# Optimization experiments

Hardware: AMD Instinct MI355X
Metric: run time of the kernel (lower is better)

## Reference

```python
import jax, jax.numpy as jnp
import numpy as np

N = 100000      # nodes
E = 1600000     # edges
D_IN = 128
D_H = 128
D_OUT = 128


def setup_inputs() -> dict:
    key = jax.random.key(0)
    ks = jax.random.split(key, 8)
    x = jax.random.normal(ks[0], (N, D_IN), dtype=jnp.float32)
    edge_index = jax.random.randint(ks[1], (2, E), 0, N, dtype=jnp.int32)
    s = 1.0 / np.sqrt(D_IN)
    W1 = jax.random.uniform(ks[2], (D_IN, D_H), jnp.float32, -s, s)
    b1 = jnp.zeros((D_H,), jnp.float32)
    W2 = jax.random.uniform(ks[3], (D_H, D_H), jnp.float32, -s, s)
    b2 = jnp.zeros((D_H,), jnp.float32)
    W3 = jax.random.uniform(ks[4], (D_H, D_OUT), jnp.float32, -s, s)
    b3 = jnp.zeros((D_OUT,), jnp.float32)
    return {"x": x, "edge_index": edge_index,
            "W1": W1, "b1": b1, "W2": W2, "b2": b2, "W3": W3, "b3": b3}


def _gcn_conv(x, W, b, src, dst, norm, n_nodes):
    # PyG GCNConv: out = scatter_add(norm * (x @ W)[src] -> dst) + b
    h = x @ W
    msg = h[src] * norm[:, None]                       # [E+N, d]
    agg = jax.ops.segment_sum(msg, dst, num_segments=n_nodes)
    return agg + b


def reference(x, edge_index, W1, b1, W2, b2, W3, b3):
    n = x.shape[0]
    loop = jnp.arange(n, dtype=edge_index.dtype)
    src = jnp.concatenate([edge_index[0], loop])       # add self-loops
    dst = jnp.concatenate([edge_index[1], loop])
    # symmetric normalization: deg computed on target (incl. self-loops)
    deg = jax.ops.segment_sum(jnp.ones_like(dst, dtype=x.dtype), dst,
                              num_segments=n)
    dis = jnp.where(deg > 0, jax.lax.rsqrt(jnp.maximum(deg, 1.0)), 0.0)
    norm = dis[src] * dis[dst]                         # [E+N]

    h = _gcn_conv(x, W1, b1, src, dst, norm, n)
    h = jax.nn.relu(h)                                 # dropout: eval mode = identity
    h = _gcn_conv(h, W2, b2, src, dst, norm, n)
    h = jax.nn.relu(h)
    out = _gcn_conv(h, W3, b3, src, dst, norm, n)
    return out
```

## Files before the change

### kernel.cpp

```cpp
#include <hip/hip_runtime.h>
#include <hip/hip_fp16.h>

#define D 128
#define TPAD 136
#define NPB 256
#define KMAX 512
#define CHUNK 4096
#define SCAP 6144
#define SRCMASK 0x1FFFF

typedef _Float16 half_t;
typedef _Float16 f16x8 __attribute__((ext_vector_type(8)));
typedef float f32x4 __attribute__((ext_vector_type(4)));


__global__ __launch_bounds__(256) void setup_kernel(const float* __restrict__ W1,
                                                    const float* __restrict__ W2,
                                                    const float* __restrict__ W3,
                                                    half_t* __restrict__ Wf1,
                                                    half_t* __restrict__ Wf2,
                                                    half_t* __restrict__ Wf3,
                                                    const int* __restrict__ dst,
                                                    int* __restrict__ bucket_cnt, int E) {
    __shared__ int scnt[KMAX];
    int b = blockIdx.x, t = threadIdx.x;
    if (b < 96) {
        const float* W = (b < 32) ? W1 : (b < 64) ? W2 : W3;
        half_t* Wf = (b < 32) ? Wf1 : (b < 64) ? Wf2 : Wf3;
        int bb = b & 31;
        int s = bb >> 3, tq = bb & 7;
        for (int e = t; e < 512; e += 256) {
            int l = e >> 3, j = e & 7;
            int k = s * 32 + ((l >> 4) & 3) * 4 + (j & 3) + ((j >> 2) << 4);
            int nn = tq * 16 + (l & 15);
            Wf[(size_t)((s * 8 + tq) * 64 + l) * 8 + j] = (half_t)W[k * 128 + nn];
        }
    } else if (b >= 98) {
        for (int i = t; i < KMAX; i += 256) scnt[i] = 0;
        __syncthreads();
        int base = (b - 98) * CHUNK;
        int nE = min(CHUNK, E - base);
        for (int i = t; i < nE; i += 256)
            atomicAdd(&scnt[dst[base + i] >> 8], 1);
        __syncthreads();
        for (int i = t; i < KMAX; i += 256)
            if (scnt[i]) atomicAdd(&bucket_cnt[i], scnt[i]);
    }
}

__global__ __launch_bounds__(KMAX) void bucket_scan_kernel(const int* __restrict__ bucket_cnt,
                                                           int* __restrict__ bucket_ptr,
                                                           int* __restrict__ bucket_cur,
                                                           int K, int E) {
    __shared__ int sh[KMAX];
    int t = threadIdx.x;
    int v = (t < K) ? bucket_cnt[t] : 0;
    sh[t] = v;
    __syncthreads();
    for (int off = 1; off < KMAX; off <<= 1) {
        int add = (t >= off) ? sh[t - off] : 0;
        __syncthreads();
        sh[t] += add;
        __syncthreads();
    }
    if (t < K) {
        int ex = sh[t] - v;
        bucket_ptr[t] = ex;
        bucket_cur[t] = ex;
    }
    if (t == 0) bucket_ptr[K] = E;
}

__global__ __launch_bounds__(256) void bucket_scatter_kernel(const int* __restrict__ src,
                                                             const int* __restrict__ dst,
                                                             int* __restrict__ bucket_cur,
                                                             int* __restrict__ bpack, int E) {
    __shared__ int sdst[CHUNK];
    __shared__ int scnt[KMAX];
    __shared__ int sbase[KMAX];
    int t = threadIdx.x;
    int base = blockIdx.x * CHUNK;
    int nE = min(CHUNK, E - base);
    for (int i = t; i < KMAX; i += 256) scnt[i] = 0;
    __syncthreads();
    for (int i = t; i < nE; i += 256) {
        int d = dst[base + i];
        sdst[i] = d;
        atomicAdd(&scnt[d >> 8], 1);
    }
    __syncthreads();
    for (int i = t; i < KMAX; i += 256) {
        int c = scnt[i];
        sbase[i] = c ? atomicAdd(&bucket_cur[i], c) : 0;
        scnt[i] = 0;
    }
    __syncthreads();
    for (int i = t; i < nE; i += 256) {
        int d = sdst[i];
        int b = d >> 8;
        int pos = sbase[b] + atomicAdd(&scnt[b], 1);
        bpack[pos] = src[base + i] | ((d & 255) << 17);
    }
}

__global__ __launch_bounds__(256) void csr_build_kernel(const int* __restrict__ bpack,
                                                        const int* __restrict__ bucket_ptr,
                                                        int* __restrict__ row_ptr,
                                                        float* __restrict__ dis,
                                                        int* __restrict__ csr_src,
                                                        int n, int E, int K) {
    __shared__ int scnt[NPB];
    __shared__ int sh[NPB];
    __shared__ int sedge[SCAP];
    int b = blockIdx.x;
    int node0 = b << 8;
    int nn = min(NPB, n - node0);
    int t = threadIdx.x;
    int p0 = bucket_ptr[b], p1 = bucket_ptr[b + 1];
    int cnt = p1 - p0;
    bool stage = (cnt <= SCAP);
    scnt[t] = 0;
    __syncthreads();
    for (int i = t; i < cnt; i += 256) {
        int e = bpack[p0 + i];
        if (stage) sedge[i] = e;
        atomicAdd(&scnt[(e >> 17) & 255], 1);
    }
    __syncthreads();
    int v = scnt[t];
    sh[t] = v;
    __syncthreads();
    for (int off = 1; off < NPB; off <<= 1) {
        int add = (t >= off) ? sh[t - off] : 0;
        __syncthreads();
        sh[t] += add;
        __syncthreads();
    }
    int rowbase = p0 + sh[t] - v;
    if (t < nn) {
        row_ptr[node0 + t] = rowbase;
        dis[node0 + t] = rsqrtf((float)(v + 1));
    }
    if (b == K - 1 && t == 0) row_ptr[n] = E;
    scnt[t] = rowbase;
    __syncthreads();
    for (int i = t; i < cnt; i += 256) {
        int e = stage ? sedge[i] : bpack[p0 + i];
        int pos = atomicAdd(&scnt[(e >> 17) & 255], 1);
        csr_src[pos] = e & SRCMASK;
    }
}


__device__ __forceinline__ void gemm_core(half_t* sA, int tid, int base,
                                          const half_t* __restrict__ Wf,
                                          const float* __restrict__ dis,
                                          half_t* __restrict__ C, int n) {
    int l = tid & 63, w = tid >> 6;
    int m = l & 15, g = l >> 4;
    const f16x8* WF = (const f16x8*)Wf;

    f16x8 wB[4][2];
#pragma unroll
    for (int s = 0; s < 4; ++s)
#pragma unroll
        for (int j = 0; j < 2; ++j)
            wB[s][j] = WF[(size_t)(s * 8 + 2 * w + j) * 64 + l];

    f32x4 acc[4][2];
#pragma unroll
    for (int rt = 0; rt < 4; ++rt)
#pragma unroll
        for (int j = 0; j < 2; ++j) acc[rt][j] = (f32x4){0.f, 0.f, 0.f, 0.f};

#pragma unroll
    for (int s = 0; s < 4; ++s) {
#pragma unroll
        for (int rt = 0; rt < 4; ++rt) {
            union { f16x8 v; float2 f2[2]; } af;
            int a_off = (rt * 16 + m) * TPAD + s * 32 + 4 * g;
            af.f2[0] = *(const float2*)&sA[a_off];
            af.f2[1] = *(const float2*)&sA[a_off + 16];
            acc[rt][0] = __builtin_amdgcn_mfma_f32_16x16x32_f16(af.v, wB[s][0], acc[rt][0], 0, 0, 0);
            acc[rt][1] = __builtin_amdgcn_mfma_f32_16x16x32_f16(af.v, wB[s][1], acc[rt][1], 0, 0, 0);
        }
    }

    float dd[4][4];
#pragma unroll
    for (int rt = 0; rt < 4; ++rt)
#pragma unroll
        for (int r = 0; r < 4; ++r) {
            int row = base + rt * 16 + 4 * g + r;
            dd[rt][r] = (row < n) ? dis[row] : 0.f;
        }
    __syncthreads();
#pragma unroll
    for (int rt = 0; rt < 4; ++rt)
#pragma unroll
        for (int j = 0; j < 2; ++j)
#pragma unroll
            for (int r = 0; r < 4; ++r)
                sA[(rt * 16 + 4 * g + r) * TPAD + (2 * w + j) * 16 + m] =
                    (half_t)(acc[rt][j][r] * dd[rt][r]);
    __syncthreads();
#pragma unroll
    for (int q = 0; q < 4; ++q) {
        int f4 = q * 256 + tid;
        int r = f4 >> 4, c = f4 & 15;
        int row = base + r;
        if (row < n)
            *(float4*)&C[(size_t)row * D + c * 8] = *(const float4*)&sA[r * TPAD + c * 8];
    }
}

__global__ __launch_bounds__(256) void gemm_mfma_f32in(const float* __restrict__ A,
                                                       const half_t* __restrict__ Wf,
                                                       const float* __restrict__ dis,
                                                       half_t* __restrict__ C, int n) {
    __shared__ half_t sA[64 * TPAD];
    int tid = threadIdx.x;
    int base = blockIdx.x * 64;

    const float4* A4 = (const float4*)A;
#pragma unroll
    for (int it = 0; it < 8; ++it) {
        int idx = it * 256 + tid;
        int r = idx >> 5, kq = idx & 31;
        int grow = base + r;
        float4 va = (grow < n) ? A4[(size_t)grow * 32 + kq]
                               : make_float4(0.f, 0.f, 0.f, 0.f);
        union { half_t h[4]; float2 f2; } pk;
        pk.h[0] = (half_t)va.x; pk.h[1] = (half_t)va.y;
        pk.h[2] = (half_t)va.z; pk.h[3] = (half_t)va.w;
        *(float2*)&sA[r * TPAD + kq * 4] = pk.f2;
    }
    __syncthreads();
    gemm_core(sA, tid, base, Wf, dis, C, n);
}

__global__ __launch_bounds__(256) void gemm_mfma_f16in(const half_t* __restrict__ A,
                                                       const half_t* __restrict__ Wf,
                                                       const float* __restrict__ dis,
                                                       half_t* __restrict__ C, int n) {
    __shared__ half_t sA[64 * TPAD];
    int tid = threadIdx.x;
    int base = blockIdx.x * 64;

    const float4* A4 = (const float4*)A;
#pragma unroll
    for (int it = 0; it < 4; ++it) {
        int idx = it * 256 + tid;
        int r = idx >> 4, c16 = idx & 15;
        int grow = base + r;
        float4 va = (grow < n) ? A4[(size_t)grow * 16 + c16]
                               : make_float4(0.f, 0.f, 0.f, 0.f);
        *(float4*)&sA[r * TPAD + c16 * 8] = va;
    }
    __syncthreads();
    gemm_core(sA, tid, base, Wf, dis, C, n);
}


template <bool F16OUT>
__global__ __launch_bounds__(256) void aggregate_kernel(const __half2* __restrict__ Hs,
                                                        const int* __restrict__ row_ptr,
                                                        const int* __restrict__ csr_src,
                                                        const float* __restrict__ dis,
                                                        const float* __restrict__ b,
                                                        void* __restrict__ outv, int n) {
    int node = blockIdx.x * 4 + (threadIdx.x >> 6);
    if (node >= n) return;
    int lane = threadIdx.x & 63;

    float2 s0 = __half22float2(Hs[(size_t)node * 64 + lane]);
    float accx = s0.x, accy = s0.y;

    int p0 = row_ptr[node], p1 = row_ptr[node + 1];
    int p = p0;
    int nb8 = (p1 - p0) >> 3;
    if (nb8 > 0) {
        int idx[8];
#pragma unroll
        for (int u = 0; u < 8; ++u) idx[u] = csr_src[p + u];
        for (int bb = 1; bb < nb8; ++bb) {
            int nxt[8];
#pragma unroll
            for (int u = 0; u < 8; ++u) nxt[u] = csr_src[p + 8 + u];
            __half2 v[8];
#pragma unroll
            for (int u = 0; u < 8; ++u) v[u] = Hs[(size_t)idx[u] * 64 + lane];
#pragma unroll
            for (int u = 0; u < 8; ++u) {
                float2 f = __half22float2(v[u]);
                accx += f.x; accy += f.y;
            }
#pragma unroll
            for (int u = 0; u < 8; ++u) idx[u] = nxt[u];
            p += 8;
        }
        {
            __half2 v[8];
#pragma unroll
            for (int u = 0; u < 8; ++u) v[u] = Hs[(size_t)idx[u] * 64 + lane];
#pragma unroll
            for (int u = 0; u < 8; ++u) {
                float2 f = __half22float2(v[u]);
                accx += f.x; accy += f.y;
            }
            p += 8;
        }
    }
    for (; p + 4 <= p1; p += 4) {
        int s0i = csr_src[p + 0];
        int s1i = csr_src[p + 1];
        int s2i = csr_src[p + 2];
        int s3i = csr_src[p + 3];
        __half2 v0 = Hs[(size_t)s0i * 64 + lane];
        __half2 v1 = Hs[(size_t)s1i * 64 + lane];
        __half2 v2 = Hs[(size_t)s2i * 64 + lane];
        __half2 v3 = Hs[(size_t)s3i * 64 + lane];
        float2 f0 = __half22float2(v0), f1 = __half22float2(v1);
        float2 f2 = __half22float2(v2), f3 = __half22float2(v3);
        accx += f0.x; accy += f0.y;
        accx += f1.x; accy += f1.y;
        accx += f2.x; accy += f2.y;
        accx += f3.x; accy += f3.y;
    }
    for (; p < p1; ++p) {
        int s = csr_src[p];
        float2 f = __half22float2(Hs[(size_t)s * 64 + lane]);
        accx += f.x; accy += f.y;
    }

    float di = dis[node];
    float2 bb2 = *(const float2*)(b + 2 * lane);
    float ox = fmaf(accx, di, bb2.x);
    float oy = fmaf(accy, di, bb2.y);
    if (F16OUT) {
        ox = fmaxf(ox, 0.f);
        oy = fmaxf(oy, 0.f);
        ((__half2*)outv)[(size_t)node * 64 + lane] = __floats2half2_rn(ox, oy);
    } else {
        float2 o; o.x = ox; o.y = oy;
        ((float2*)((float*)outv + (size_t)node * D))[lane] = o;
    }
}


extern "C" void kernel_launch(void* const* d_in, const int* in_sizes, int n_in,
                              void* d_out, int out_size, void* d_ws, size_t ws_size,
                              hipStream_t stream) {
    const float* x  = (const float*)d_in[0];
    const int*   ei = (const int*)d_in[1];
    const float* W1 = (const float*)d_in[2];
    const float* b1 = (const float*)d_in[3];
    const float* W2 = (const float*)d_in[4];
    const float* b2 = (const float*)d_in[5];
    const float* W3 = (const float*)d_in[6];
    const float* b3 = (const float*)d_in[7];
    float* out = (float*)d_out;

    int n = in_sizes[0] / D;
    int E = in_sizes[1] / 2;
    const int* src = ei;
    const int* dst = ei + E;
    int K = (n + NPB - 1) >> 8;

    char* ws = (char*)d_ws;
    half_t* hbuf     = (half_t*)ws; ws += (size_t)n * D * sizeof(half_t);
    half_t* outh     = (half_t*)ws; ws += (size_t)n * D * sizeof(half_t);
    float* dis       = (float*)ws;  ws += (size_t)n * sizeof(float);
    int* row_ptr     = (int*)ws;    ws += (size_t)(n + 1) * sizeof(int);
    int* csr_src     = (int*)ws;    ws += (size_t)E * sizeof(int);
    int* bucket_cnt  = (int*)ws;    ws += KMAX * sizeof(int);
    int* bucket_ptr  = (int*)ws;    ws += (KMAX + 1) * sizeof(int);
    int* bucket_cur  = (int*)ws;    ws += KMAX * sizeof(int);
    ws = (char*)(((uintptr_t)ws + 15) & ~(uintptr_t)15);
    half_t* Wf1      = (half_t*)ws; ws += 128 * 128 * sizeof(half_t);
    half_t* Wf2      = (half_t*)ws; ws += 128 * 128 * sizeof(half_t);
    half_t* Wf3      = (half_t*)ws; ws += 128 * 128 * sizeof(half_t);
    int* bpack       = (int*)hbuf;

    int gC = (E + CHUNK - 1) / CHUNK;
    int gM = (n + 63) / 64;
    int gA = (n + 3) / 4;

    hipMemsetAsync(bucket_cnt, 0, KMAX * sizeof(int), stream);
    setup_kernel<<<98 + gC, 256, 0, stream>>>(W1, W2, W3, Wf1, Wf2, Wf3,
                                              dst, bucket_cnt, E);
    bucket_scan_kernel<<<1, KMAX, 0, stream>>>(bucket_cnt, bucket_ptr, bucket_cur, K, E);
    bucket_scatter_kernel<<<gC, 256, 0, stream>>>(src, dst, bucket_cur, bpack, E);
    csr_build_kernel<<<K, 256, 0, stream>>>(bpack, bucket_ptr, row_ptr, dis, csr_src, n, E, K);

    gemm_mfma_f32in<<<gM, 256, 0, stream>>>(x, Wf1, dis, hbuf, n);
    aggregate_kernel<true><<<gA, 256, 0, stream>>>((const __half2*)hbuf, row_ptr, csr_src, dis, b1, outh, n);
    gemm_mfma_f16in<<<gM, 256, 0, stream>>>(outh, Wf2, dis, hbuf, n);
    aggregate_kernel<true><<<gA, 256, 0, stream>>>((const __half2*)hbuf, row_ptr, csr_src, dis, b2, outh, n);
    gemm_mfma_f16in<<<gM, 256, 0, stream>>>(outh, Wf3, dis, hbuf, n);
    aggregate_kernel<false><<<gA, 256, 0, stream>>>((const __half2*)hbuf, row_ptr, csr_src, dis, b3, out, n);
}
```

Before: 415.9 us.

## Fuse first GEMM into bucket scatter kernel, moving source-degree scaling into aggregation

Measured after the change: 433.7 us. 1.04x slower.

```diff
diff --git a/kernel.cpp b/kernel.cpp
--- a/kernel.cpp
+++ b/kernel.cpp
@@ -71,35 +71,127 @@
     if (t == 0) bucket_ptr[K] = E;
 }
 
-__global__ __launch_bounds__(256) void bucket_scatter_kernel(const int* __restrict__ src,
-                                                             const int* __restrict__ dst,
-                                                             int* __restrict__ bucket_cur,
-                                                             int* __restrict__ bpack, int E) {
-    __shared__ int sdst[CHUNK];
-    __shared__ int scnt[KMAX];
-    __shared__ int sbase[KMAX];
+
+template <bool SCALE>
+__device__ __forceinline__ void gemm_core(half_t* sA, int tid, int base,
+                                          const half_t* __restrict__ Wf,
+                                          const float* __restrict__ dis,
+                                          half_t* __restrict__ C, int n) {
+    int l = tid & 63, w = tid >> 6;
+    int m = l & 15, g = l >> 4;
+    const f16x8* WF = (const f16x8*)Wf;
+
+    f16x8 wB[4][2];
+#pragma unroll
+    for (int s = 0; s < 4; ++s)
+#pragma unroll
+        for (int j = 0; j < 2; ++j)
+            wB[s][j] = WF[(size_t)(s * 8 + 2 * w + j) * 64 + l];
+
+    f32x4 acc[4][2];
+#pragma unroll
+    for (int rt = 0; rt < 4; ++rt)
+#pragma unroll
+        for (int j = 0; j < 2; ++j) acc[rt][j] = (f32x4){0.f, 0.f, 0.f, 0.f};
+
+#pragma unroll
+    for (int s = 0; s < 4; ++s) {
+#pragma unroll
+        for (int rt = 0; rt < 4; ++rt) {
+            union { f16x8 v; float2 f2[2]; } af;
+            int a_off = (rt * 16 + m) * TPAD + s * 32 + 4 * g;
+            af.f2[0] = *(const float2*)&sA[a_off];
+            af.f2[1] = *(const float2*)&sA[a_off + 16];
+            acc[rt][0] = __builtin_amdgcn_mfma_f32_16x16x32_f16(af.v, wB[s][0], acc[rt][0], 0, 0, 0);
+            acc[rt][1] = __builtin_amdgcn_mfma_f32_16x16x32_f16(af.v, wB[s][1], acc[rt][1], 0, 0, 0);
+        }
+    }
+
+    float dd[4][4];
+#pragma unroll
+    for (int rt = 0; rt < 4; ++rt)
+#pragma unroll
+        for (int r = 0; r < 4; ++r) {
+            int row = base + rt * 16 + 4 * g + r;
+            dd[rt][r] = SCALE ? ((row < n) ? dis[row] : 0.f) : 1.f;
+        }
+    __syncthreads();
+#pragma unroll
+    for (int rt = 0; rt < 4; ++rt)
+#pragma unroll
+        for (int j = 0; j < 2; ++j)
+#pragma unroll
+            for (int r = 0; r < 4; ++r)
+                sA[(rt * 16 + 4 * g + r) * TPAD + (2 * w + j) * 16 + m] =
+                    (half_t)(acc[rt][j][r] * dd[rt][r]);
+    __syncthreads();
+#pragma unroll
+    for (int q = 0; q < 4; ++q) {
+        int f4 = q * 256 + tid;
+        int r = f4 >> 4, c = f4 & 15;
+        int row = base + r;
+        if (row < n)
+            *(float4*)&C[(size_t)row * D + c * 8] = *(const float4*)&sA[r * TPAD + c * 8];
+    }
+}
+
+
+__global__ __launch_bounds__(256) void scatter_gemm_kernel(const int* __restrict__ src,
+                                                           const int* __restrict__ dst,
+                                                           int* __restrict__ bucket_cur,
+                                                           int* __restrict__ bpack, int E,
+                                                           const float* __restrict__ A,
+                                                           const half_t* __restrict__ Wf,
+                                                           half_t* __restrict__ C, int n,
+                                                           int gC) {
+    __shared__ __align__(16) char smem[20480];
     int t = threadIdx.x;
-    int base = blockIdx.x * CHUNK;
-    int nE = min(CHUNK, E - base);
-    for (int i = t; i < KMAX; i += 256) scnt[i] = 0;
-    __syncthreads();
-    for (int i = t; i < nE; i += 256) {
-        int d = dst[base + i];
-        sdst[i] = d;
-        atomicAdd(&scnt[d >> 8], 1);
-    }
-    __syncthreads();
-    for (int i = t; i < KMAX; i += 256) {
-        int c = scnt[i];
-        sbase[i] = c ? atomicAdd(&bucket_cur[i], c) : 0;
-        scnt[i] = 0;
-    }
-    __syncthreads();
-    for (int i = t; i < nE; i += 256) {
-        int d = sdst[i];
-        int b = d >> 8;
-        int pos = sbase[b] + atomicAdd(&scnt[b], 1);
-        bpack[pos] = src[base + i] | ((d & 255) << 17);
+    int b = blockIdx.x;
+
+    if (b < gC) {
+        int* sdst = (int*)smem;
+        int* scnt = (int*)(smem + 16384);
+        int* sbase = (int*)(smem + 18432);
+        int base = b * CHUNK;
+        int nE = min(CHUNK, E - base);
+        for (int i = t; i < KMAX; i += 256) scnt[i] = 0;
+        __syncthreads();
+        for (int i = t; i < nE; i += 256) {
+            int d = dst[base + i];
+            sdst[i] = d;
+            atomicAdd(&scnt[d >> 8], 1);
+        }
+        __syncthreads();
+        for (int i = t; i < KMAX; i += 256) {
+            int c = scnt[i];
+            sbase[i] = c ? atomicAdd(&bucket_cur[i], c) : 0;
+            scnt[i] = 0;
+        }
+        __syncthreads();
+        for (int i = t; i < nE; i += 256) {
+            int d = sdst[i];
+            int bk = d >> 8;
+            int pos = sbase[bk] + atomicAdd(&scnt[bk], 1);
+            bpack[pos] = src[base + i] | ((d & 255) << 17);
+        }
+    } else {
+        half_t* sA = (half_t*)smem;
+        int gbase = (b - gC) * 64;
+        const float4* A4 = (const float4*)A;
+#pragma unroll
+        for (int it = 0; it < 8; ++it) {
+            int idx = it * 256 + t;
+            int r = idx >> 5, kq = idx & 31;
+            int grow = gbase + r;
+            float4 va = (grow < n) ? A4[(size_t)grow * 32 + kq]
+                                   : make_float4(0.f, 0.f, 0.f, 0.f);
+            union { half_t h[4]; float2 f2; } pk;
+            pk.h[0] = (half_t)va.x; pk.h[1] = (half_t)va.y;
+            pk.h[2] = (half_t)va.z; pk.h[3] = (half_t)va.w;
+            *(float2*)&sA[r * TPAD + kq * 4] = pk.f2;
+        }
+        __syncthreads();
+        gemm_core<false>(sA, t, gbase, Wf, nullptr, C, n);
     }
 }
 
@@ -151,94 +243,6 @@
     }
 }
 
-
-__device__ __forceinline__ void gemm_core(half_t* sA, int tid, int base,
-                                          const half_t* __restrict__ Wf,
-                                          const float* __restrict__ dis,
-                                          half_t* __restrict__ C, int n) {
-    int l = tid & 63, w = tid >> 6;
-    int m = l & 15, g = l >> 4;
-    const f16x8* WF = (const f16x8*)Wf;
-
-    f16x8 wB[4][2];
-#pragma unroll
-    for (int s = 0; s < 4; ++s)
-#pragma unroll
-        for (int j = 0; j < 2; ++j)
-            wB[s][j] = WF[(size_t)(s * 8 + 2 * w + j) * 64 + l];
-
-    f32x4 acc[4][2];
-#pragma unroll
-    for (int rt = 0; rt < 4; ++rt)
-#pragma unroll
-        for (int j = 0; j < 2; ++j) acc[rt][j] = (f32x4){0.f, 0.f, 0.f, 0.f};
-
-#pragma unroll
-    for (int s = 0; s < 4; ++s) {
-#pragma unroll
-        for (int rt = 0; rt < 4; ++rt) {
-            union { f16x8 v; float2 f2[2]; } af;
-            int a_off = (rt * 16 + m) * TPAD + s * 32 + 4 * g;
-            af.f2[0] = *(const float2*)&sA[a_off];
-            af.f2[1] = *(const float2*)&sA[a_off + 16];
-            acc[rt][0] = __builtin_amdgcn_mfma_f32_16x16x32_f16(af.v, wB[s][0], acc[rt][0], 0, 0, 0);
-            acc[rt][1] = __builtin_amdgcn_mfma_f32_16x16x32_f16(af.v, wB[s][1], acc[rt][1], 0, 0, 0);
-        }
-    }
-
-    float dd[4][4];
-#pragma unroll
-    for (int rt = 0; rt < 4; ++rt)
-#pragma unroll
-        for (int r = 0; r < 4; ++r) {
-            int row = base + rt * 16 + 4 * g + r;
-            dd[rt][r] = (row < n) ? dis[row] : 0.f;
-        }
-    __syncthreads();
-#pragma unroll
-    for (int rt = 0; rt < 4; ++rt)
-#pragma unroll
-        for (int j = 0; j < 2; ++j)
-#pragma unroll
-            for (int r = 0; r < 4; ++r)
-                sA[(rt * 16 + 4 * g + r) * TPAD + (2 * w + j) * 16 + m] =
-                    (half_t)(acc[rt][j][r] * dd[rt][r]);
-    __syncthreads();
-#pragma unroll
-    for (int q = 0; q < 4; ++q) {
-        int f4 = q * 256 + tid;
-        int r = f4 >> 4, c = f4 & 15;
-        int row = base + r;
-        if (row < n)
-            *(float4*)&C[(size_t)row * D + c * 8] = *(const float4*)&sA[r * TPAD + c * 8];
-    }
-}
-
-__global__ __launch_bounds__(256) void gemm_mfma_f32in(const float* __restrict__ A,
-                                                       const half_t* __restrict__ Wf,
-                                                       const float* __restrict__ dis,
-                                                       half_t* __restrict__ C, int n) {
-    __shared__ half_t sA[64 * TPAD];
-    int tid = threadIdx.x;
-    int base = blockIdx.x * 64;
-
-    const float4* A4 = (const float4*)A;
-#pragma unroll
-    for (int it = 0; it < 8; ++it) {
-        int idx = it * 256 + tid;
-        int r = idx >> 5, kq = idx & 31;
-        int grow = base + r;
-        float4 va = (grow < n) ? A4[(size_t)grow * 32 + kq]
-                               : make_float4(0.f, 0.f, 0.f, 0.f);
-        union { half_t h[4]; float2 f2; } pk;
-        pk.h[0] = (half_t)va.x; pk.h[1] = (half_t)va.y;
-        pk.h[2] = (half_t)va.z; pk.h[3] = (half_t)va.w;
-        *(float2*)&sA[r * TPAD + kq * 4] = pk.f2;
-    }
-    __syncthreads();
-    gemm_core(sA, tid, base, Wf, dis, C, n);
-}
-
 __global__ __launch_bounds__(256) void gemm_mfma_f16in(const half_t* __restrict__ A,
                                                        const half_t* __restrict__ Wf,
                                                        const float* __restrict__ dis,
@@ -258,11 +262,11 @@
         *(float4*)&sA[r * TPAD + c16 * 8] = va;
     }
     __syncthreads();
-    gemm_core(sA, tid, base, Wf, dis, C, n);
-}
-
-
-template <bool F16OUT>
+    gemm_core<true>(sA, tid, base, Wf, dis, C, n);
+}
+
+
+template <bool F16OUT, bool EDGESCALE>
 __global__ __launch_bounds__(256) void aggregate_kernel(const __half2* __restrict__ Hs,
                                                         const int* __restrict__ row_ptr,
                                                         const int* __restrict__ csr_src,
@@ -273,8 +277,10 @@
     if (node >= n) return;
     int lane = threadIdx.x & 63;
 
+    float di = dis[node];
     float2 s0 = __half22float2(Hs[(size_t)node * 64 + lane]);
-    float accx = s0.x, accy = s0.y;
+    float selfs = EDGESCALE ? di : 1.f;
+    float accx = selfs * s0.x, accy = selfs * s0.y;
 
     int p0 = row_ptr[node], p1 = row_ptr[node + 1];
     int p = p0;
@@ -288,12 +294,17 @@
 #pragma unroll
             for (int u = 0; u < 8; ++u) nxt[u] = csr_src[p + 8 + u];
             __half2 v[8];
-#pragma unroll
-            for (int u = 0; u < 8; ++u) v[u] = Hs[(size_t)idx[u] * 64 + lane];
+            float sc[8];
+#pragma unroll
+            for (int u = 0; u < 8; ++u) {
+                v[u] = Hs[(size_t)idx[u] * 64 + lane];
+                sc[u] = EDGESCALE ? dis[idx[u]] : 1.f;
+            }
 #pragma unroll
             for (int u = 0; u < 8; ++u) {
                 float2 f = __half22float2(v[u]);
-                accx += f.x; accy += f.y;
+                if (EDGESCALE) { accx = fmaf(sc[u], f.x, accx); accy = fmaf(sc[u], f.y, accy); }
+                else           { accx += f.x; accy += f.y; }
             }
 #pragma unroll
             for (int u = 0; u < 8; ++u) idx[u] = nxt[u];
@@ -301,39 +312,29 @@
         }
         {
             __half2 v[8];
-#pragma unroll
-            for (int u = 0; u < 8; ++u) v[u] = Hs[(size_t)idx[u] * 64 + lane];
+            float sc[8];
+#pragma unroll
+            for (int u = 0; u < 8; ++u) {
+                v[u] = Hs[(size_t)idx[u] * 64 + lane];
+                sc[u] = EDGESCALE ? dis[idx[u]] : 1.f;
+            }
 #pragma unroll
             for (int u = 0; u < 8; ++u) {
                 float2 f = __half22float2(v[u]);
-                accx += f.x; accy += f.y;
+                if (EDGESCALE) { accx = fmaf(sc[u], f.x, accx); accy = fmaf(sc[u], f.y, accy); }
+                else           { accx += f.x; accy += f.y; }
             }
             p += 8;
         }
-    }
-    for (; p + 4 <= p1; p += 4) {
-        int s0i = csr_src[p + 0];
-        int s1i = csr_src[p + 1];
-        int s2i = csr_src[p + 2];
-        int s3i = csr_src[p + 3];
-        __half2 v0 = Hs[(size_t)s0i * 64 + lane];
-        __half2 v1 = Hs[(size_t)s1i * 64 + lane];
-        __half2 v2 = Hs[(size_t)s2i * 64 + lane];
-        __half2 v3 = Hs[(size_t)s3i * 64 + lane];
-        float2 f0 = __half22float2(v0), f1 = __half22float2(v1);
-        float2 f2 = __half22float2(v2), f3 = __half22float2(v3);
-        accx += f0.x; accy += f0.y;
-        accx += f1.x; accy += f1.y;
-        accx += f2.x; accy += f2.y;
-        accx += f3.x; accy += f3.y;
     }
     for (; p < p1; ++p) {
         int s = csr_src[p];
         float2 f = __half22float2(Hs[(size_t)s * 64 + lane]);
-        accx += f.x; accy += f.y;
-    }
-
-    float di = dis[node];
+        float sc = EDGESCALE ? dis[s] : 1.f;
+        if (EDGESCALE) { accx = fmaf(sc, f.x, accx); accy = fmaf(sc, f.y, accy); }
+        else           { accx += f.x; accy += f.y; }
+    }
+
     float2 bb2 = *(const float2*)(b + 2 * lane);
     float ox = fmaf(accx, di, bb2.x);
     float oy = fmaf(accy, di, bb2.y);
@@ -380,7 +381,7 @@
     half_t* Wf1      = (half_t*)ws; ws += 128 * 128 * sizeof(half_t);
     half_t* Wf2      = (half_t*)ws; ws += 128 * 128 * sizeof(half_t);
     half_t* Wf3      = (half_t*)ws; ws += 128 * 128 * sizeof(half_t);
-    int* bpack       = (int*)hbuf;
+    int* bpack       = (int*)outh;
 
     int gC = (E + CHUNK - 1) / CHUNK;
     int gM = (n + 63) / 64;
@@ -390,13 +391,13 @@
     setup_kernel<<<98 + gC, 256, 0, stream>>>(W1, W2, W3, Wf1, Wf2, Wf3,
                                               dst, bucket_cnt, E);
     bucket_scan_kernel<<<1, KMAX, 0, stream>>>(bucket_cnt, bucket_ptr, bucket_cur, K, E);
-    bucket_scatter_kernel<<<gC, 256, 0, stream>>>(src, dst, bucket_cur, bpack, E);
+    scatter_gemm_kernel<<<gC + gM, 256, 0, stream>>>(src, dst, bucket_cur, bpack, E,
+                                                     x, Wf1, hbuf, n, gC);
     csr_build_kernel<<<K, 256, 0, stream>>>(bpack, bucket_ptr, row_ptr, dis, csr_src, n, E, K);
 
-    gemm_mfma_f32in<<<gM, 256, 0, stream>>>(x, Wf1, dis, hbuf, n);
-    aggregate_kernel<true><<<gA, 256, 0, stream>>>((const __half2*)hbuf, row_ptr, csr_src, dis, b1, outh, n);
+    aggregate_kernel<true, true><<<gA, 256, 0, stream>>>((const __half2*)hbuf, row_ptr, csr_src, dis, b1, outh, n);
     gemm_mfma_f16in<<<gM, 256, 0, stream>>>(outh, Wf2, dis, hbuf, n);
-    aggregate_kernel<true><<<gA, 256, 0, stream>>>((const __half2*)hbuf, row_ptr, csr_src, dis, b2, outh, n);
+    aggregate_kernel<true, false><<<gA, 256, 0, stream>>>((const __half2*)hbuf, row_ptr, csr_src, dis, b2, outh, n);
     gemm_mfma_f16in<<<gM, 256, 0, stream>>>(outh, Wf3, dis, hbuf, n);
-    aggregate_kernel<false><<<gA, 256, 0, stream>>>((const __half2*)hbuf, row_ptr, csr_src, dis, b3, out, n);
-}
+    aggregate_kernel<false, false><<<gA, 256, 0, stream>>>((const __half2*)hbuf, row_ptr, csr_src, dis, b3, out, n);
+}
```

## Split CSR build into count pass and fuse fill with first GEMM

Applied to the files above, without the earlier changes.

Measured after the change: 405.5 us, median of 2. 2.5% less time.

```diff
diff --git a/kernel.cpp b/kernel.cpp
--- a/kernel.cpp
+++ b/kernel.cpp
@@ -6,7 +6,6 @@
 #define NPB 256
 #define KMAX 512
 #define CHUNK 4096
-#define SCAP 6144
 #define SRCMASK 0x1FFFF
 
 typedef _Float16 half_t;
@@ -103,29 +102,22 @@
     }
 }
 
-__global__ __launch_bounds__(256) void csr_build_kernel(const int* __restrict__ bpack,
+__global__ __launch_bounds__(256) void csr_count_kernel(const int* __restrict__ bpack,
                                                         const int* __restrict__ bucket_ptr,
                                                         int* __restrict__ row_ptr,
                                                         float* __restrict__ dis,
-                                                        int* __restrict__ csr_src,
                                                         int n, int E, int K) {
     __shared__ int scnt[NPB];
     __shared__ int sh[NPB];
-    __shared__ int sedge[SCAP];
     int b = blockIdx.x;
     int node0 = b << 8;
     int nn = min(NPB, n - node0);
     int t = threadIdx.x;
+    scnt[t] = 0;
+    __syncthreads();
     int p0 = bucket_ptr[b], p1 = bucket_ptr[b + 1];
-    int cnt = p1 - p0;
-    bool stage = (cnt <= SCAP);
-    scnt[t] = 0;
-    __syncthreads();
-    for (int i = t; i < cnt; i += 256) {
-        int e = bpack[p0 + i];
-        if (stage) sedge[i] = e;
-        atomicAdd(&scnt[(e >> 17) & 255], 1);
-    }
+    for (int i = p0 + t; i < p1; i += 256)
+        atomicAdd(&scnt[(bpack[i] >> 17) & 255], 1);
     __syncthreads();
     int v = scnt[t];
     sh[t] = v;
@@ -136,22 +128,15 @@
         sh[t] += add;
         __syncthreads();
     }
-    int rowbase = p0 + sh[t] - v;
     if (t < nn) {
-        row_ptr[node0 + t] = rowbase;
+        row_ptr[node0 + t] = p0 + sh[t] - v;
         dis[node0 + t] = rsqrtf((float)(v + 1));
     }
     if (b == K - 1 && t == 0) row_ptr[n] = E;
-    scnt[t] = rowbase;
-    __syncthreads();
-    for (int i = t; i < cnt; i += 256) {
-        int e = stage ? sedge[i] : bpack[p0 + i];
-        int pos = atomicAdd(&scnt[(e >> 17) & 255], 1);
-        csr_src[pos] = e & SRCMASK;
-    }
-}
-
-
+}
+
+
+template <bool SCALE>
 __device__ __forceinline__ void gemm_core(half_t* sA, int tid, int base,
                                           const half_t* __restrict__ Wf,
                                           const float* __restrict__ dis,
@@ -192,7 +177,7 @@
 #pragma unroll
         for (int r = 0; r < 4; ++r) {
             int row = base + rt * 16 + 4 * g + r;
-            dd[rt][r] = (row < n) ? dis[row] : 0.f;
+            dd[rt][r] = SCALE ? ((row < n) ? dis[row] : 0.f) : 1.f;
         }
     __syncthreads();
 #pragma unroll
@@ -214,29 +199,49 @@
     }
 }
 
-__global__ __launch_bounds__(256) void gemm_mfma_f32in(const float* __restrict__ A,
-                                                       const half_t* __restrict__ Wf,
-                                                       const float* __restrict__ dis,
-                                                       half_t* __restrict__ C, int n) {
-    __shared__ half_t sA[64 * TPAD];
-    int tid = threadIdx.x;
-    int base = blockIdx.x * 64;
-
-    const float4* A4 = (const float4*)A;
-#pragma unroll
-    for (int it = 0; it < 8; ++it) {
-        int idx = it * 256 + tid;
-        int r = idx >> 5, kq = idx & 31;
-        int grow = base + r;
-        float4 va = (grow < n) ? A4[(size_t)grow * 32 + kq]
-                               : make_float4(0.f, 0.f, 0.f, 0.f);
-        union { half_t h[4]; float2 f2; } pk;
-        pk.h[0] = (half_t)va.x; pk.h[1] = (half_t)va.y;
-        pk.h[2] = (half_t)va.z; pk.h[3] = (half_t)va.w;
-        *(float2*)&sA[r * TPAD + kq * 4] = pk.f2;
-    }
-    __syncthreads();
-    gemm_core(sA, tid, base, Wf, dis, C, n);
+
+__global__ __launch_bounds__(256) void fill_gemm_kernel(const int* __restrict__ bpack,
+                                                        const int* __restrict__ bucket_ptr,
+                                                        const int* __restrict__ row_ptr,
+                                                        int* __restrict__ csr_src, int K,
+                                                        const float* __restrict__ A,
+                                                        const half_t* __restrict__ Wf,
+                                                        const float* __restrict__ dis,
+                                                        half_t* __restrict__ C, int n) {
+    __shared__ __align__(16) char smem[64 * TPAD * sizeof(half_t)];
+    int b = blockIdx.x, t = threadIdx.x;
+
+    if (b < K) {
+        int* cursor = (int*)smem;
+        int node0 = b << 8;
+        int nn = min(NPB, n - node0);
+        if (t < nn) cursor[t] = row_ptr[node0 + t];
+        __syncthreads();
+        int p0 = bucket_ptr[b], p1 = bucket_ptr[b + 1];
+        for (int i = p0 + t; i < p1; i += 256) {
+            int e = bpack[i];
+            int pos = atomicAdd(&cursor[(e >> 17) & 255], 1);
+            csr_src[pos] = e & SRCMASK;
+        }
+    } else {
+        half_t* sA = (half_t*)smem;
+        int base = (b - K) * 64;
+        const float4* A4 = (const float4*)A;
+#pragma unroll
+        for (int it = 0; it < 8; ++it) {
+            int idx = it * 256 + t;
+            int r = idx >> 5, kq = idx & 31;
+            int grow = base + r;
+            float4 va = (grow < n) ? A4[(size_t)grow * 32 + kq]
+                                   : make_float4(0.f, 0.f, 0.f, 0.f);
+            union { half_t h[4]; float2 f2; } pk;
+            pk.h[0] = (half_t)va.x; pk.h[1] = (half_t)va.y;
+            pk.h[2] = (half_t)va.z; pk.h[3] = (half_t)va.w;
+            *(float2*)&sA[r * TPAD + kq * 4] = pk.f2;
+        }
+        __syncthreads();
+        gemm_core<true>(sA, t, base, Wf, dis, C, n);
+    }
 }
 
 __global__ __launch_bounds__(256) void gemm_mfma_f16in(const half_t* __restrict__ A,
@@ -258,7 +263,7 @@
         *(float4*)&sA[r * TPAD + c16 * 8] = va;
     }
     __syncthreads();
-    gemm_core(sA, tid, base, Wf, dis, C, n);
+    gemm_core<true>(sA, tid, base, Wf, dis, C, n);
 }
 
 
@@ -380,7 +385,7 @@
     half_t* Wf1      = (half_t*)ws; ws += 128 * 128 * sizeof(half_t);
     half_t* Wf2      = (half_t*)ws; ws += 128 * 128 * sizeof(half_t);
     half_t* Wf3      = (half_t*)ws; ws += 128 * 128 * sizeof(half_t);
-    int* bpack       = (int*)hbuf;
+    int* bpack       = (int*)outh;
 
     int gC = (E + CHUNK - 1) / CHUNK;
     int gM = (n + 63) / 64;
@@ -391,9 +396,10 @@
                                               dst, bucket_cnt, E);
     bucket_scan_kernel<<<1, KMAX, 0, stream>>>(bucket_cnt, bucket_ptr, bucket_cur, K, E);
     bucket_scatter_kernel<<<gC, 256, 0, stream>>>(src, dst, bucket_cur, bpack, E);
-    csr_build_kernel<<<K, 256, 0, stream>>>(bpack, bucket_ptr, row_ptr, dis, csr_src, n, E, K);
-
-    gemm_mfma_f32in<<<gM, 256, 0, stream>>>(x, Wf1, dis, hbuf, n);
+    csr_count_kernel<<<K, 256, 0, stream>>>(bpack, bucket_ptr, row_ptr, dis, n, E, K);
+    fill_gemm_kernel<<<K + gM, 256, 0, stream>>>(bpack, bucket_ptr, row_ptr, csr_src, K,
+                                                 x, Wf1, dis, hbuf, n);
+
     aggregate_kernel<true><<<gA, 256, 0, stream>>>((const __half2*)hbuf, row_ptr, csr_src, dis, b1, outh, n);
     gemm_mfma_f16in<<<gM, 256, 0, stream>>>(outh, Wf2, dis, hbuf, n);
     aggregate_kernel<true><<<gA, 256, 0, stream>>>((const __half2*)hbuf, row_ptr, csr_src, dis, b2, outh, n);
```

## Compute degrees early and co-launch layer-1 GEMM with bucket scatter

Applied to the files above, without the earlier changes.

Measured after the change: 458.8 us. 10.3% more time.

```diff
diff --git a/kernel.cpp b/kernel.cpp
--- a/kernel.cpp
+++ b/kernel.cpp
@@ -21,7 +21,8 @@
                                                     half_t* __restrict__ Wf2,
                                                     half_t* __restrict__ Wf3,
                                                     const int* __restrict__ dst,
-                                                    int* __restrict__ bucket_cnt, int E) {
+                                                    int* __restrict__ bucket_cnt,
+                                                    int* __restrict__ deg, int E) {
     __shared__ int scnt[KMAX];
     int b = blockIdx.x, t = threadIdx.x;
     if (b < 96) {
@@ -40,73 +41,175 @@
         __syncthreads();
         int base = (b - 98) * CHUNK;
         int nE = min(CHUNK, E - base);
-        for (int i = t; i < nE; i += 256)
-            atomicAdd(&scnt[dst[base + i] >> 8], 1);
+        for (int i = t; i < nE; i += 256) {
+            int d = dst[base + i];
+            atomicAdd(&scnt[d >> 8], 1);
+            atomicAdd(&deg[d], 1);
+        }
         __syncthreads();
         for (int i = t; i < KMAX; i += 256)
             if (scnt[i]) atomicAdd(&bucket_cnt[i], scnt[i]);
     }
 }
 
-__global__ __launch_bounds__(KMAX) void bucket_scan_kernel(const int* __restrict__ bucket_cnt,
-                                                           int* __restrict__ bucket_ptr,
+__global__ __launch_bounds__(KMAX) void scan_dis_kernel(const int* __restrict__ bucket_cnt,
+                                                        int* __restrict__ bucket_ptr,
+                                                        int* __restrict__ bucket_cur,
+                                                        const int* __restrict__ deg,
+                                                        float* __restrict__ dis,
+                                                        int K, int E, int n) {
+    __shared__ int sh[KMAX];
+    int t = threadIdx.x, b = blockIdx.x;
+    if (b == 0) {
+        int v = (t < K) ? bucket_cnt[t] : 0;
+        sh[t] = v;
+        __syncthreads();
+        for (int off = 1; off < KMAX; off <<= 1) {
+            int add = (t >= off) ? sh[t - off] : 0;
+            __syncthreads();
+            sh[t] += add;
+            __syncthreads();
+        }
+        if (t < K) {
+            int ex = sh[t] - v;
+            bucket_ptr[t] = ex;
+            bucket_cur[t] = ex;
+        }
+        if (t == 0) bucket_ptr[K] = E;
+    } else {
+        int i = (b - 1) * KMAX + t;
+        if (i < n) dis[i] = rsqrtf((float)(deg[i] + 1));
+    }
+}
+
+
+template <bool SCALE>
+__device__ __forceinline__ void gemm_core(half_t* sA, int tid, int base,
+                                          const half_t* __restrict__ Wf,
+                                          const float* __restrict__ dis,
+                                          half_t* __restrict__ C, int n) {
+    int l = tid & 63, w = tid >> 6;
+    int m = l & 15, g = l >> 4;
+    const f16x8* WF = (const f16x8*)Wf;
+
+    f16x8 wB[4][2];
+#pragma unroll
+    for (int s = 0; s < 4; ++s)
+#pragma unroll
+        for (int j = 0; j < 2; ++j)
+            wB[s][j] = WF[(size_t)(s * 8 + 2 * w + j) * 64 + l];
+
+    f32x4 acc[4][2];
+#pragma unroll
+    for (int rt = 0; rt < 4; ++rt)
+#pragma unroll
+        for (int j = 0; j < 2; ++j) acc[rt][j] = (f32x4){0.f, 0.f, 0.f, 0.f};
+
+#pragma unroll
+    for (int s = 0; s < 4; ++s) {
+#pragma unroll
+        for (int rt = 0; rt < 4; ++rt) {
+            union { f16x8 v; float2 f2[2]; } af;
+            int a_off = (rt * 16 + m) * TPAD + s * 32 + 4 * g;
+            af.f2[0] = *(const float2*)&sA[a_off];
+            af.f2[1] = *(const float2*)&sA[a_off + 16];
+            acc[rt][0] = __builtin_amdgcn_mfma_f32_16x16x32_f16(af.v, wB[s][0], acc[rt][0], 0, 0, 0);
+            acc[rt][1] = __builtin_amdgcn_mfma_f32_16x16x32_f16(af.v, wB[s][1], acc[rt][1], 0, 0, 0);
+        }
+    }
+
+    float dd[4][4];
+#pragma unroll
+    for (int rt = 0; rt < 4; ++rt)
+#pragma unroll
+        for (int r = 0; r < 4; ++r) {
+            int row = base + rt * 16 + 4 * g + r;
+            dd[rt][r] = SCALE ? ((row < n) ? dis[row] : 0.f) : 1.f;
+        }
+    __syncthreads();
+#pragma unroll
+    for (int rt = 0; rt < 4; ++rt)
+#pragma unroll
+        for (int j = 0; j < 2; ++j)
+#pragma unroll
+            for (int r = 0; r < 4; ++r)
+                sA[(rt * 16 + 4 * g + r) * TPAD + (2 * w + j) * 16 + m] =
+                    (half_t)(acc[rt][j][r] * dd[rt][r]);
+    __syncthreads();
+#pragma unroll
+    for (int q = 0; q < 4; ++q) {
+        int f4 = q * 256 + tid;
+        int r = f4 >> 4, c = f4 & 15;
+        int row = base + r;
+        if (row < n)
+            *(float4*)&C[(size_t)row * D + c * 8] = *(const float4*)&sA[r * TPAD + c * 8];
+    }
+}
+
+
+__global__ __launch_bounds__(256) void scatter_gemm_kernel(const int* __restrict__ src,
+                                                           const int* __restrict__ dst,
                                                            int* __restrict__ bucket_cur,
-                                                           int K, int E) {
-    __shared__ int sh[KMAX];
+                                                           int* __restrict__ bpack, int E,
+                                                           const float* __restrict__ A,
+                                                           const half_t* __restrict__ Wf,
+                                                           const float* __restrict__ dis,
+                                                           half_t* __restrict__ C, int n,
+                                                           int gC) {
+    __shared__ __align__(16) char smem[20480];
     int t = threadIdx.x;
-    int v = (t < K) ? bucket_cnt[t] : 0;
-    sh[t] = v;
-    __syncthreads();
-    for (int off = 1; off < KMAX; off <<= 1) {
-        int add = (t >= off) ? sh[t - off] : 0;
-        __syncthreads();
-        sh[t] += add;
-        __syncthreads();
-    }
-    if (t < K) {
-        int ex = sh[t] - v;
-        bucket_ptr[t] = ex;
-        bucket_cur[t] = ex;
-    }
-    if (t == 0) bucket_ptr[K] = E;
-}
-
-__global__ __launch_bounds__(256) void bucket_scatter_kernel(const int* __restrict__ src,
-                                                             const int* __restrict__ dst,
-                                                             int* __restrict__ bucket_cur,
-                                                             int* __restrict__ bpack, int E) {
-    __shared__ int sdst[CHUNK];
-    __shared__ int scnt[KMAX];
-    __shared__ int sbase[KMAX];
-    int t = threadIdx.x;
-    int base = blockIdx.x * CHUNK;
-    int nE = min(CHUNK, E - base);
-    for (int i = t; i < KMAX; i += 256) scnt[i] = 0;
-    __syncthreads();
-    for (int i = t; i < nE; i += 256) {
-        int d = dst[base + i];
-        sdst[i] = d;
-        atomicAdd(&scnt[d >> 8], 1);
-    }
-    __syncthreads();
-    for (int i = t; i < KMAX; i += 256) {
-        int c = scnt[i];
-        sbase[i] = c ? atomicAdd(&bucket_cur[i], c) : 0;
-        scnt[i] = 0;
-    }
-    __syncthreads();
-    for (int i = t; i < nE; i += 256) {
-        int d = sdst[i];
-        int b = d >> 8;
-        int pos = sbase[b] + atomicAdd(&scnt[b], 1);
-        bpack[pos] = src[base + i] | ((d & 255) << 17);
+    int b = blockIdx.x;
+
+    if (b < gC) {
+        int* sdst = (int*)smem;
+        int* scnt = (int*)(smem + 16384);
+        int* sbase = (int*)(smem + 18432);
+        int base = b * CHUNK;
+        int nE = min(CHUNK, E - base);
+        for (int i = t; i < KMAX; i += 256) scnt[i] = 0;
+        __syncthreads();
+        for (int i = t; i < nE; i += 256) {
+            int d = dst[base + i];
+            sdst[i] = d;
+            atomicAdd(&scnt[d >> 8], 1);
+        }
+        __syncthreads();
+        for (int i = t; i < KMAX; i += 256) {
+            int c = scnt[i];
+            sbase[i] = c ? atomicAdd(&bucket_cur[i], c) : 0;
+            scnt[i] = 0;
+        }
+        __syncthreads();
+        for (int i = t; i < nE; i += 256) {
+            int d = sdst[i];
+            int bk = d >> 8;
+            int pos = sbase[bk] + atomicAdd(&scnt[bk], 1);
+            bpack[pos] = src[base + i] | ((d & 255) << 17);
+        }
+    } else {
+        half_t* sA = (half_t*)smem;
+        int gbase = (b - gC) * 64;
+        const float4* A4 = (const float4*)A;
+#pragma unroll
+        for (int it = 0; it < 8; ++it) {
+            int idx = it * 256 + t;
+            int r = idx >> 5, kq = idx & 31;
+            int grow = gbase + r;
+            float4 va = (grow < n) ? A4[(size_t)grow * 32 + kq]
+                                   : make_float4(0.f, 0.f, 0.f, 0.f);
+            union { half_t h[4]; float2 f2; } pk;
+            pk.h[0] = (half_t)va.x; pk.h[1] = (half_t)va.y;
+            pk.h[2] = (half_t)va.z; pk.h[3] = (half_t)va.w;
+            *(float2*)&sA[r * TPAD + kq * 4] = pk.f2;
+        }
+        __syncthreads();
+        gemm_core<true>(sA, t, gbase, Wf, dis, C, n);
     }
 }
 
 __global__ __launch_bounds__(256) void csr_build_kernel(const int* __restrict__ bpack,
                                                         const int* __restrict__ bucket_ptr,
                                                         int* __restrict__ row_ptr,
-                                                        float* __restrict__ dis,
                                                         int* __restrict__ csr_src,
                                                         int n, int E, int K) {
     __shared__ int scnt[NPB];
@@ -137,10 +240,7 @@
         __syncthreads();
     }
     int rowbase = p0 + sh[t] - v;
-    if (t < nn) {
-        row_ptr[node0 + t] = rowbase;
-        dis[node0 + t] = rsqrtf((float)(v + 1));
-    }
+    if (t < nn) row_ptr[node0 + t] = rowbase;
     if (b == K - 1 && t == 0) row_ptr[n] = E;
     scnt[t] = rowbase;
     __syncthreads();
@@ -149,94 +249,6 @@
         int pos = atomicAdd(&scnt[(e >> 17) & 255], 1);
         csr_src[pos] = e & SRCMASK;
     }
-}
-
-
-__device__ __forceinline__ void gemm_core(half_t* sA, int tid, int base,
-                                          const half_t* __restrict__ Wf,
-                                          const float* __restrict__ dis,
-                                          half_t* __restrict__ C, int n) {
-    int l = tid & 63, w = tid >> 6;
-    int m = l & 15, g = l >> 4;
-    const f16x8* WF = (const f16x8*)Wf;
-
-    f16x8 wB[4][2];
-#pragma unroll
-    for (int s = 0; s < 4; ++s)
-#pragma unroll
-        for (int j = 0; j < 2; ++j)
-            wB[s][j] = WF[(size_t)(s * 8 + 2 * w + j) * 64 + l];
-
-    f32x4 acc[4][2];
-#pragma unroll
-    for (int rt = 0; rt < 4; ++rt)
-#pragma unroll
-        for (int j = 0; j < 2; ++j) acc[rt][j] = (f32x4){0.f, 0.f, 0.f, 0.f};
-
-#pragma unroll
-    for (int s = 0; s < 4; ++s) {
-#pragma unroll
-        for (int rt = 0; rt < 4; ++rt) {
-            union { f16x8 v; float2 f2[2]; } af;
-            int a_off = (rt * 16 + m) * TPAD + s * 32 + 4 * g;
-            af.f2[0] = *(const float2*)&sA[a_off];
-            af.f2[1] = *(const float2*)&sA[a_off + 16];
-            acc[rt][0] = __builtin_amdgcn_mfma_f32_16x16x32_f16(af.v, wB[s][0], acc[rt][0], 0, 0, 0);
-            acc[rt][1] = __builtin_amdgcn_mfma_f32_16x16x32_f16(af.v, wB[s][1], acc[rt][1], 0, 0, 0);
-        }
-    }
-
-    float dd[4][4];
-#pragma unroll
-    for (int rt = 0; rt < 4; ++rt)
-#pragma unroll
-        for (int r = 0; r < 4; ++r) {
-            int row = base + rt * 16 + 4 * g + r;
-            dd[rt][r] = (row < n) ? dis[row] : 0.f;
-        }
-    __syncthreads();
-#pragma unroll
-    for (int rt = 0; rt < 4; ++rt)
-#pragma unroll
-        for (int j = 0; j < 2; ++j)
-#pragma unroll
-            for (int r = 0; r < 4; ++r)
-                sA[(rt * 16 + 4 * g + r) * TPAD + (2 * w + j) * 16 + m] =
-                    (half_t)(acc[rt][j][r] * dd[rt][r]);
-    __syncthreads();
-#pragma unroll
-    for (int q = 0; q < 4; ++q) {
-        int f4 = q * 256 + tid;
-        int r = f4 >> 4, c = f4 & 15;
-        int row = base + r;
-        if (row < n)
-            *(float4*)&C[(size_t)row * D + c * 8] = *(const float4*)&sA[r * TPAD + c * 8];
-    }
-}
-
-__global__ __launch_bounds__(256) void gemm_mfma_f32in(const float* __restrict__ A,
-                                                       const half_t* __restrict__ Wf,
-                                                       const float* __restrict__ dis,
-                                                       half_t* __restrict__ C, int n) {
-    __shared__ half_t sA[64 * TPAD];
-    int tid = threadIdx.x;
-    int base = blockIdx.x * 64;
-
-    const float4* A4 = (const float4*)A;
-#pragma unroll
-    for (int it = 0; it < 8; ++it) {
-        int idx = it * 256 + tid;
-        int r = idx >> 5, kq = idx & 31;
-        int grow = base + r;
-        float4 va = (grow < n) ? A4[(size_t)grow * 32 + kq]
-                               : make_float4(0.f, 0.f, 0.f, 0.f);
-        union { half_t h[4]; float2 f2; } pk;
-        pk.h[0] = (half_t)va.x; pk.h[1] = (half_t)va.y;
-        pk.h[2] = (half_t)va.z; pk.h[3] = (half_t)va.w;
-        *(float2*)&sA[r * TPAD + kq * 4] = pk.f2;
-    }
-    __syncthreads();
-    gemm_core(sA, tid, base, Wf, dis, C, n);
 }
 
 __global__ __launch_bounds__(256) void gemm_mfma_f16in(const half_t* __restrict__ A,
@@ -258,7 +270,7 @@
         *(float4*)&sA[r * TPAD + c16 * 8] = va;
     }
     __syncthreads();
-    gemm_core(sA, tid, base, Wf, dis, C, n);
+    gemm_core<true>(sA, tid, base, Wf, dis, C, n);
 }
 
 
@@ -374,26 +386,29 @@
     int* row_ptr     = (int*)ws;    ws += (size_t)(n + 1) * sizeof(int);
     int* csr_src     = (int*)ws;    ws += (size_t)E * sizeof(int);
     int* bucket_cnt  = (int*)ws;    ws += KMAX * sizeof(int);
+    int* deg         = (int*)ws;    ws += (size_t)n * sizeof(int);
     int* bucket_ptr  = (int*)ws;    ws += (KMAX + 1) * sizeof(int);
     int* bucket_cur  = (int*)ws;    ws += KMAX * sizeof(int);
     ws = (char*)(((uintptr_t)ws + 15) & ~(uintptr_t)15);
     half_t* Wf1      = (half_t*)ws; ws += 128 * 128 * sizeof(half_t);
     half_t* Wf2      = (half_t*)ws; ws += 128 * 128 * sizeof(half_t);
     half_t* Wf3      = (half_t*)ws; ws += 128 * 128 * sizeof(half_t);
-    int* bpack       = (int*)hbuf;
+    int* bpack       = (int*)outh;
 
     int gC = (E + CHUNK - 1) / CHUNK;
     int gM = (n + 63) / 64;
     int gA = (n + 3) / 4;
-
-    hipMemsetAsync(bucket_cnt, 0, KMAX * sizeof(int), stream);
+    int gS = 1 + (n + KMAX - 1) / KMAX;
+
+    hipMemsetAsync(bucket_cnt, 0, (size_t)(KMAX + n) * sizeof(int), stream);
     setup_kernel<<<98 + gC, 256, 0, stream>>>(W1, W2, W3, Wf1, Wf2, Wf3,
-                                              dst, bucket_cnt, E);
-    bucket_scan_kernel<<<1, KMAX, 0, stream>>>(bucket_cnt, bucket_ptr, bucket_cur, K, E);
-    bucket_scatter_kernel<<<gC, 256, 0, stream>>>(src, dst, bucket_cur, bpack, E);
-    csr_build_kernel<<<K, 256, 0, stream>>>(bpack, bucket_ptr, row_ptr, dis, csr_src, n, E, K);
-
-    gemm_mfma_f32in<<<gM, 256, 0, stream>>>(x, Wf1, dis, hbuf, n);
+                                              dst, bucket_cnt, deg, E);
+    scan_dis_kernel<<<gS, KMAX, 0, stream>>>(bucket_cnt, bucket_ptr, bucket_cur,
+                                             deg, dis, K, E, n);
+    scatter_gemm_kernel<<<gC + gM, 256, 0, stream>>>(src, dst, bucket_cur, bpack, E,
+                                                     x, Wf1, dis, hbuf, n, gC);
+    csr_build_kernel<<<K, 256, 0, stream>>>(bpack, bucket_ptr, row_ptr, csr_src, n, E, K);
+
     aggregate_kernel<true><<<gA, 256, 0, stream>>>((const __half2*)hbuf, row_ptr, csr_src, dis, b1, outh, n);
     gemm_mfma_f16in<<<gM, 256, 0, stream>>>(outh, Wf2, dis, hbuf, n);
     aggregate_kernel<true><<<gA, 256, 0, stream>>>((const __half2*)hbuf, row_ptr, csr_src, dis, b2, outh, n);
```
